# Kernel optimization log

Measured on AMD Instinct MI355X. Metric: run time of the kernel, lower is better.

The kernel has to match this reference:

```python
import jax, jax.numpy as jnp
import numpy as np

N = 50000        # nodes
E = 800000       # edges (avg degree 16)
F_NODE = 128     # node feature dim
F_EDGE = 8       # edge feature dim
H_ATT = 64       # attention hidden dim
H = 8            # attention heads
P = 16           # propagation dim per head (H*P = 128)


def setup_inputs() -> dict:
    key = jax.random.key(0)
    ks = jax.random.split(key, 16)
    s = lambda fan_in: 1.0 / np.sqrt(fan_in)
    return {
        "feat": jax.random.normal(ks[0], (N, F_NODE), jnp.float32),
        "feat_edge": jax.random.normal(ks[1], (E, F_EDGE), jnp.float32),
        "src": jax.random.randint(ks[2], (E,), 0, N, jnp.int32),
        "dst": jax.random.randint(ks[3], (E,), 0, N, jnp.int32),
        # attention MLPs (no bias), stored as [in, out]
        "w_att_src0": jax.random.normal(ks[4], (F_NODE, H_ATT), jnp.float32) * s(F_NODE),
        "w_att_src1": jax.random.normal(ks[5], (H_ATT, H), jnp.float32) * s(H_ATT),
        "w_att_dst0": jax.random.normal(ks[6], (F_NODE, H_ATT), jnp.float32) * s(F_NODE),
        "w_att_dst1": jax.random.normal(ks[7], (H_ATT, H), jnp.float32) * s(H_ATT),
        "w_att_edge0": jax.random.normal(ks[8], (F_EDGE, H_ATT), jnp.float32) * s(F_EDGE),
        "w_att_edge1": jax.random.normal(ks[9], (H_ATT, H), jnp.float32) * s(H_ATT),
        # propagation projections (single layer: Linear(F_NODE, H*P) with bias)
        "w_prop_src": jax.random.normal(ks[10], (F_NODE, H * P), jnp.float32) * s(F_NODE),
        "b_prop_src": jnp.zeros((H * P,), jnp.float32),
        "w_prop_dst": jax.random.normal(ks[11], (F_NODE, H * P), jnp.float32) * s(F_NODE),
        "b_prop_dst": jnp.zeros((H * P,), jnp.float32),
    }


def reference(feat, feat_edge, src, dst,
              w_att_src0, w_att_src1, w_att_dst0, w_att_dst1,
              w_att_edge0, w_att_edge1,
              w_prop_src, b_prop_src, w_prop_dst, b_prop_dst):
    relu = jax.nn.relu
    n = feat.shape[0]

    # propagation branch: [N, H*P] -> [N, H, P]
    prop_src = (feat @ w_prop_src + b_prop_src).reshape(n, H, P)
    prop_dst = (feat @ w_prop_dst + b_prop_dst).reshape(n, H, P)

    # attention MLPs -> per-node / per-edge head logits [*, H]
    a_src = relu(feat @ w_att_src0) @ w_att_src1          # [N, H]
    a_dst = relu(feat @ w_att_dst0) @ w_att_dst1          # [N, H]
    a_edge = relu(feat_edge @ w_att_edge0) @ w_att_edge1  # [E, H]

    # per-edge attention logit: relu(a_src[u] + a_dst[v] + a_edge)
    att = relu(a_src[src] + a_dst[dst] + a_edge)          # [E, H]

    # edge softmax over incoming edges of each destination node (per head)
    m = jax.ops.segment_max(att, dst, num_segments=n)     # [N, H]
    ex = jnp.exp(att - m[dst])                            # [E, H]
    denom = jax.ops.segment_sum(ex, dst, num_segments=n)  # [N, H]
    alpha = ex / jnp.maximum(denom[dst], 1e-16)           # [E, H]

    # message = prop_src[u] * alpha, sum-aggregate to destinations
    msg = prop_src[src] * alpha[:, :, None]               # [E, H, P]
    agg = jax.ops.segment_sum(msg, dst, num_segments=n)   # [N, H, P]

    # n_hiddens_agg == []: residual add of prop_dst
    return agg + prop_dst
```

## Files before the change

kernel.cpp:

```cpp
#include <hip/hip_runtime.h>
#include <hip/hip_bf16.h>

#define NODECAP 48
#define NPB 256
#define BCAP 4608
#define MAXBUCK 256
#define PART_CHUNK 1600
#define EPART_BLOCKS 500
#define SLICES 8

typedef __attribute__((ext_vector_type(8))) short bf16x8;
typedef __attribute__((ext_vector_type(4))) float f32x4;

static __device__ __forceinline__ short f2b(float f) {
    __hip_bfloat16 h = __float2bfloat16(f);
    return *reinterpret_cast<short*>(&h);
}
static __device__ __forceinline__ float b2f(unsigned short u) {
    union { unsigned int i; float f; } v; v.i = ((unsigned int)u) << 16; return v.f;
}

__global__ __launch_bounds__(256) void pack_w(
    const float* __restrict__ w_ps, const float* __restrict__ w_pd,
    const float* __restrict__ w_as0, const float* __restrict__ w_ad0,
    short* __restrict__ wp, short* __restrict__ wa, int* __restrict__ gcnt, int nbuck)
{
    const int idx = blockIdx.x * 256 + threadIdx.x;
    if (idx < 256 * 128) {
        const int c = idx >> 7, k = idx & 127;
        const float v = (c < 128) ? w_ps[(size_t)k * 128 + c] : w_pd[(size_t)k * 128 + (c - 128)];
        wp[idx] = f2b(v);
    } else if (idx < 256 * 128 + 128 * 128) {
        const int j = idx - 256 * 128;
        const int c = j >> 7, k = j & 127;
        const float v = (c < 64) ? w_as0[(size_t)k * 64 + c] : w_ad0[(size_t)k * 64 + (c - 64)];
        wa[j] = f2b(v);
    }
    if (idx < nbuck) gcnt[idx] = 0;
}

__global__ __launch_bounds__(256) void node_mfma(
    const float* __restrict__ feat,
    const short* __restrict__ wp, const short* __restrict__ wa,
    const float* __restrict__ b_ps, const float* __restrict__ b_pd,
    const float* __restrict__ w_as1, const float* __restrict__ w_ad1,
    short* __restrict__ prop_bf, short* __restrict__ pd_bf,
    short* __restrict__ a_src_bf, float* __restrict__ a_dst, int n)
{
    __shared__ unsigned char afb[64 * 256];
    __shared__ short ht[64][137];
    const int t = threadIdx.x;
    const int lane = t & 63;
    const int wid = t >> 6;
    const int l15 = lane & 15;
    const int l4 = lane >> 4;
    const int base = blockIdx.x * 64;

    #pragma unroll
    for (int i = 0; i < 4; ++i) {
        const int chunk = t + i * 256;
        const int row = chunk >> 4;
        const int kc = chunk & 15;
        const int grow = base + row;
        float f[8];
        if (grow < n) {
            const float4 v0 = *reinterpret_cast<const float4*>(feat + (size_t)grow * 128 + kc * 8);
            const float4 v1 = *reinterpret_cast<const float4*>(feat + (size_t)grow * 128 + kc * 8 + 4);
            f[0] = v0.x; f[1] = v0.y; f[2] = v0.z; f[3] = v0.w;
            f[4] = v1.x; f[5] = v1.y; f[6] = v1.z; f[7] = v1.w;
        } else {
            #pragma unroll
            for (int j = 0; j < 8; ++j) f[j] = 0.f;
        }
        short h8[8];
        #pragma unroll
        for (int j = 0; j < 8; ++j) h8[j] = f2b(f[j]);
        const int byte = (row * 256 + kc * 16) ^ ((row & 7) << 4);
        *reinterpret_cast<bf16x8*>(afb + byte) = *reinterpret_cast<const bf16x8*>(h8);
    }
    __syncthreads();

    {
        f32x4 acc[4][4] = {};
        for (int kk = 0; kk < 4; ++kk) {
            bf16x8 a[4], b[4];
            #pragma unroll
            for (int rt = 0; rt < 4; ++rt) {
                const int arow = rt * 16 + l15;
                const int ab = (arow * 256 + kk * 64 + l4 * 16) ^ ((arow & 7) << 4);
                a[rt] = *reinterpret_cast<const bf16x8*>(afb + ab);
            }
            #pragma unroll
            for (int c = 0; c < 4; ++c) {
                const int col = (wid * 4 + c) * 16 + l15;
                b[c] = *reinterpret_cast<const bf16x8*>(wp + (size_t)col * 128 + kk * 32 + l4 * 8);
            }
            #pragma unroll
            for (int rt = 0; rt < 4; ++rt)
                #pragma unroll
                for (int c = 0; c < 4; ++c)
                    acc[rt][c] = __builtin_amdgcn_mfma_f32_16x16x32_bf16(a[rt], b[c], acc[rt][c], 0, 0, 0);
        }
        #pragma unroll
        for (int c = 0; c < 4; ++c) {
            const int col = (wid * 4 + c) * 16 + l15;
            const bool sr = (col < 128);
            const float bias = sr ? b_ps[col] : b_pd[col - 128];
            short* dbase = sr ? (prop_bf + col) : (pd_bf + (col - 128));
            #pragma unroll
            for (int rt = 0; rt < 4; ++rt)
                #pragma unroll
                for (int r = 0; r < 4; ++r) {
                    const int row = base + rt * 16 + l4 * 4 + r;
                    if (row < n) dbase[(size_t)row * 128] = f2b(acc[rt][c][r] + bias);
                }
        }
    }

    {
        f32x4 acc[4][2] = {};
        for (int kk = 0; kk < 4; ++kk) {
            bf16x8 a[4], b[2];
            #pragma unroll
            for (int rt = 0; rt < 4; ++rt) {
                const int arow = rt * 16 + l15;
                const int ab = (arow * 256 + kk * 64 + l4 * 16) ^ ((arow & 7) << 4);
                a[rt] = *reinterpret_cast<const bf16x8*>(afb + ab);
            }
            #pragma unroll
            for (int c = 0; c < 2; ++c) {
                const int col = (wid * 2 + c) * 16 + l15;
                b[c] = *reinterpret_cast<const bf16x8*>(wa + (size_t)col * 128 + kk * 32 + l4 * 8);
            }
            #pragma unroll
            for (int rt = 0; rt < 4; ++rt)
                #pragma unroll
                for (int c = 0; c < 2; ++c)
                    acc[rt][c] = __builtin_amdgcn_mfma_f32_16x16x32_bf16(a[rt], b[c], acc[rt][c], 0, 0, 0);
        }
        #pragma unroll
        for (int c = 0; c < 2; ++c) {
            const int col = (wid * 2 + c) * 16 + l15;
            #pragma unroll
            for (int rt = 0; rt < 4; ++rt)
                #pragma unroll
                for (int r = 0; r < 4; ++r)
                    ht[rt * 16 + l4 * 4 + r][col] = f2b(fmaxf(acc[rt][c][r], 0.f));
        }
    }
    __syncthreads();

    #pragma unroll
    for (int o = 0; o < 4; ++o) {
        const int idx = t + o * 256;
        const int i = idx >> 4;
        const int hh = idx & 15;
        const bool is_src = (hh < 8);
        const int h = is_src ? hh : (hh - 8);
        const float* w1 = is_src ? w_as1 : w_ad1;
        const int jb = is_src ? 0 : 64;
        float acc = 0.f;
        #pragma unroll
        for (int j = 0; j < 64; ++j)
            acc += b2f((unsigned short)ht[i][jb + j]) * w1[j * 8 + h];
        const int row = base + i;
        if (row < n) {
            if (is_src) a_src_bf[(size_t)row * 8 + h] = f2b(acc);
            else        a_dst[(size_t)row * 8 + h] = acc;
        }
    }
}

__global__ __launch_bounds__(256) void edge_part(
    const int* __restrict__ src, const int* __restrict__ dst,
    const float* __restrict__ feat_edge,
    const float* __restrict__ w_e0, const float* __restrict__ w_e1,
    const short* __restrict__ a_src_bf,
    int* __restrict__ gcnt, int2* __restrict__ part, short* __restrict__ ax,
    int E, int nbuck)
{
    __shared__ int hist[MAXBUCK];
    __shared__ int cursor[MAXBUCK];
    __shared__ int dcache[PART_CHUNK];
    const int t = threadIdx.x;

    if (blockIdx.x < EPART_BLOCKS) {
        const int e0 = blockIdx.x * PART_CHUNK;
        const int e1 = min(e0 + PART_CHUNK, E);

        for (int i = t; i < nbuck; i += 256) hist[i] = 0;
        __syncthreads();
        for (int e = e0 + t; e < e1; e += 256) {
            const int d = dst[e];
            dcache[e - e0] = d;
            atomicAdd(&hist[d >> 8], 1);
        }
        __syncthreads();
        for (int i = t; i < nbuck; i += 256) {
            const int c = hist[i];
            cursor[i] = (c > 0) ? atomicAdd(&gcnt[i], c) : 0;
        }
        __syncthreads();
        for (int e = e0 + t; e < e1; e += 256) {
            const int d = dcache[e - e0];
            const int s = src[e];
            const int b = d >> 8;
            const int pos = atomicAdd(&cursor[b], 1);
            if (pos < BCAP)
                part[(size_t)b * BCAP + pos] = make_int2((e << 8) | (d & 255), s);
        }
        return;
    }

    const int e = (blockIdx.x - EPART_BLOCKS) * 256 + t;
    if (e >= E) return;

    float fe[8];
    const float4 v0 = *reinterpret_cast<const float4*>(feat_edge + (size_t)e * 8);
    const float4 v1 = *reinterpret_cast<const float4*>(feat_edge + (size_t)e * 8 + 4);
    fe[0] = v0.x; fe[1] = v0.y; fe[2] = v0.z; fe[3] = v0.w;
    fe[4] = v1.x; fe[5] = v1.y; fe[6] = v1.z; fe[7] = v1.w;

    float ae[8] = {};
    #pragma unroll 8
    for (int j = 0; j < 64; ++j) {
        float hj = 0.f;
        #pragma unroll
        for (int k = 0; k < 8; ++k) hj += fe[k] * w_e0[k * 64 + j];
        hj = fmaxf(hj, 0.f);
        #pragma unroll
        for (int hh = 0; hh < 8; ++hh) ae[hh] += hj * w_e1[j * 8 + hh];
    }

    const int s = src[e];
    const ushort4 as0 = *reinterpret_cast<const ushort4*>(a_src_bf + (size_t)s * 8);
    const ushort4 as1 = *reinterpret_cast<const ushort4*>(a_src_bf + (size_t)s * 8 + 4);
    short eb[8];
    eb[0] = f2b(ae[0] + b2f(as0.x)); eb[1] = f2b(ae[1] + b2f(as0.y));
    eb[2] = f2b(ae[2] + b2f(as0.z)); eb[3] = f2b(ae[3] + b2f(as0.w));
    eb[4] = f2b(ae[4] + b2f(as1.x)); eb[5] = f2b(ae[5] + b2f(as1.y));
    eb[6] = f2b(ae[6] + b2f(as1.z)); eb[7] = f2b(ae[7] + b2f(as1.w));
    *reinterpret_cast<uint4*>(ax + (size_t)e * 8) = *reinterpret_cast<const uint4*>(eb);
}

__global__ __launch_bounds__(256) void bucket_agg(
    const int2* __restrict__ part, const int* __restrict__ gcnt,
    const short* __restrict__ ax, const float* __restrict__ a_dst,
    const short* __restrict__ prop_bf, const short* __restrict__ pd_bf,
    float* __restrict__ out, int n)
{
    __shared__ int2  lists[32][NODECAP];
    __shared__ int   lcnt[32];
    __shared__ float adst_s[32][8];
    const int t = threadIdx.x;
    const int b = blockIdx.x >> 3;
    const int slice = blockIdx.x & 7;
    const int node0 = (b << 8) + (slice << 5);

    if (t < 32) lcnt[t] = 0;
    {
        const int r = t >> 3, h = t & 7;
        const int nd = node0 + r;
        adst_s[r][h] = (nd < n) ? a_dst[(size_t)nd * 8 + h] : 0.f;
    }
    __syncthreads();

    const int cnt = min(gcnt[b], BCAP);
    const int2* pb = part + (size_t)b * BCAP;
    for (int j = t; j < cnt; j += 256) {
        const int2 pr = pb[j];
        const int dlow = pr.x & 255;
        if ((dlow >> 5) == slice) {
            const int r = dlow & 31;
            const int slot = atomicAdd(&lcnt[r], 1);
            if (slot < NODECAP) lists[r][slot] = make_int2(pr.x >> 8, pr.y);
        }
    }
    __syncthreads();

    const int grp = t >> 5, l = t & 31;
    const int h = l >> 2, q = l & 3;

    for (int r = grp; r < 32; r += 8) {
        const int node = node0 + r;
        if (node >= n) continue;
        int deg = lcnt[r];
        if (deg > NODECAP) deg = NODECAP;
        const float adv = adst_s[r][h];

        float dsumv = 0.f;
        float4 acc = make_float4(0.f, 0.f, 0.f, 0.f);
        for (int j0 = 0; j0 < deg; j0 += 8) {
            float at[8]; float4 pv[8];
            #pragma unroll
            for (int u = 0; u < 8; ++u) {
                const int j = j0 + u;
                const bool act = (j < deg);
                const int2 pr = lists[r][act ? j : 0];
                at[u] = b2f((unsigned short)ax[(size_t)pr.x * 8 + h]);
                const ushort4 p = *reinterpret_cast<const ushort4*>(
                    prop_bf + (size_t)pr.y * 128 + h * 16 + q * 4);
                pv[u] = make_float4(b2f(p.x), b2f(p.y), b2f(p.z), b2f(p.w));
            }
            #pragma unroll
            for (int u = 0; u < 8; ++u) {
                const bool act = (j0 + u < deg);
                const float ex = act ? __expf(fmaxf(at[u] + adv, 0.f)) : 0.f;
                dsumv += ex;
                acc.x += ex * pv[u].x; acc.y += ex * pv[u].y;
                acc.z += ex * pv[u].z; acc.w += ex * pv[u].w;
            }
        }
        const float dinv = 1.f / fmaxf(dsumv, 1e-16f);

        const ushort4 pd = *reinterpret_cast<const ushort4*>(
            pd_bf + (size_t)node * 128 + h * 16 + q * 4);
        float4 o;
        o.x = b2f(pd.x) + acc.x * dinv; o.y = b2f(pd.y) + acc.y * dinv;
        o.z = b2f(pd.z) + acc.z * dinv; o.w = b2f(pd.w) + acc.w * dinv;
        *reinterpret_cast<float4*>(out + (size_t)node * 128 + h * 16 + q * 4) = o;
    }
}

extern "C" void kernel_launch(void* const* d_in, const int* in_sizes, int n_in,
                              void* d_out, int out_size, void* d_ws, size_t ws_size,
                              hipStream_t stream)
{
    const float* feat      = (const float*)d_in[0];
    const float* feat_edge = (const float*)d_in[1];
    const int*   src       = (const int*)d_in[2];
    const int*   dst       = (const int*)d_in[3];
    const float* w_as0     = (const float*)d_in[4];
    const float* w_as1     = (const float*)d_in[5];
    const float* w_ad0     = (const float*)d_in[6];
    const float* w_ad1     = (const float*)d_in[7];
    const float* w_e0      = (const float*)d_in[8];
    const float* w_e1      = (const float*)d_in[9];
    const float* w_ps      = (const float*)d_in[10];
    const float* b_ps      = (const float*)d_in[11];
    const float* w_pd      = (const float*)d_in[12];
    const float* b_pd      = (const float*)d_in[13];

    const int n = in_sizes[0] / 128;
    const int E = in_sizes[2];
    const int nbuck = (n + NPB - 1) / NPB;
    float* out = (float*)d_out;

    short* prop_bf = (short*)d_ws;
    short* pd_bf   = prop_bf + (size_t)n * 128;
    short* a_src_bf = pd_bf + (size_t)n * 128;
    float* a_dst = (float*)(a_src_bf + (size_t)n * 8);
    int*   gcnt  = (int*)(a_dst + (size_t)n * 8);
    int2*  part  = (int2*)(gcnt + ((nbuck + 1) & ~1));
    short* ax    = (short*)(part + (size_t)nbuck * BCAP);
    short* wp    = ax + (size_t)E * 8;
    short* wa    = wp + 256 * 128;

    pack_w<<<192, 256, 0, stream>>>(
        w_ps, w_pd, w_as0, w_ad0, wp, wa, gcnt, nbuck);

    node_mfma<<<(n + 63) / 64, 256, 0, stream>>>(
        feat, wp, wa, b_ps, b_pd, w_as1, w_ad1,
        prop_bf, pd_bf, a_src_bf, a_dst, n);

    const int axBlocks = (E + 255) / 256;
    edge_part<<<EPART_BLOCKS + axBlocks, 256, 0, stream>>>(
        src, dst, feat_edge, w_e0, w_e1, a_src_bf, gcnt, part, ax, E, nbuck);

    bucket_agg<<<nbuck * SLICES, 256, 0, stream>>>(
        part, gcnt, ax, a_dst, prop_bf, pd_bf, out, n);
}
```

Baseline: 150.4 us.

## Merge node projection and edge partition kernels into one launch

```diff
diff --git a/kernel.cpp b/kernel.cpp
--- a/kernel.cpp
+++ b/kernel.cpp
@@ -6,7 +6,6 @@
 #define BCAP 4608
 #define MAXBUCK 256
 #define PART_CHUNK 1600
-#define EPART_BLOCKS 500
 #define SLICES 8
 
 typedef __attribute__((ext_vector_type(8))) short bf16x8;
@@ -39,17 +38,80 @@
     if (idx < nbuck) gcnt[idx] = 0;
 }
 
-__global__ __launch_bounds__(256) void node_mfma(
+__global__ __launch_bounds__(256) void node_edge_part(
     const float* __restrict__ feat,
     const short* __restrict__ wp, const short* __restrict__ wa,
     const float* __restrict__ b_ps, const float* __restrict__ b_pd,
     const float* __restrict__ w_as1, const float* __restrict__ w_ad1,
     short* __restrict__ prop_bf, short* __restrict__ pd_bf,
-    short* __restrict__ a_src_bf, float* __restrict__ a_dst, int n)
+    short* __restrict__ a_src_bf, float* __restrict__ a_dst,
+    const int* __restrict__ src, const int* __restrict__ dst,
+    const float* __restrict__ feat_edge,
+    const float* __restrict__ w_e0, const float* __restrict__ w_e1,
+    int* __restrict__ gcnt, int2* __restrict__ part, short* __restrict__ ae,
+    int n, int E, int nbuck, int nodeB, int partB)
 {
-    __shared__ unsigned char afb[64 * 256];
-    __shared__ short ht[64][137];
+    __shared__ char smraw[64 * 256 + 64 * 137 * 2];
     const int t = threadIdx.x;
+
+    if (blockIdx.x >= nodeB + partB) {
+        const int e = (blockIdx.x - nodeB - partB) * 256 + t;
+        if (e >= E) return;
+        float fe[8];
+        const float4 v0 = *reinterpret_cast<const float4*>(feat_edge + (size_t)e * 8);
+        const float4 v1 = *reinterpret_cast<const float4*>(feat_edge + (size_t)e * 8 + 4);
+        fe[0] = v0.x; fe[1] = v0.y; fe[2] = v0.z; fe[3] = v0.w;
+        fe[4] = v1.x; fe[5] = v1.y; fe[6] = v1.z; fe[7] = v1.w;
+        float av[8] = {};
+        #pragma unroll 8
+        for (int j = 0; j < 64; ++j) {
+            float hj = 0.f;
+            #pragma unroll
+            for (int k = 0; k < 8; ++k) hj += fe[k] * w_e0[k * 64 + j];
+            hj = fmaxf(hj, 0.f);
+            #pragma unroll
+            for (int hh = 0; hh < 8; ++hh) av[hh] += hj * w_e1[j * 8 + hh];
+        }
+        short eb[8];
+        #pragma unroll
+        for (int hh = 0; hh < 8; ++hh) eb[hh] = f2b(av[hh]);
+        *reinterpret_cast<uint4*>(ae + (size_t)e * 8) = *reinterpret_cast<const uint4*>(eb);
+        return;
+    }
+
+    if (blockIdx.x >= nodeB) {
+        int* hist   = (int*)smraw;
+        int* cursor = hist + MAXBUCK;
+        int* dcache = cursor + MAXBUCK;
+        const int e0 = (blockIdx.x - nodeB) * PART_CHUNK;
+        const int e1 = min(e0 + PART_CHUNK, E);
+
+        for (int i = t; i < nbuck; i += 256) hist[i] = 0;
+        __syncthreads();
+        for (int e = e0 + t; e < e1; e += 256) {
+            const int d = dst[e];
+            dcache[e - e0] = d;
+            atomicAdd(&hist[d >> 8], 1);
+        }
+        __syncthreads();
+        for (int i = t; i < nbuck; i += 256) {
+            const int c = hist[i];
+            cursor[i] = (c > 0) ? atomicAdd(&gcnt[i], c) : 0;
+        }
+        __syncthreads();
+        for (int e = e0 + t; e < e1; e += 256) {
+            const int d = dcache[e - e0];
+            const int s = src[e];
+            const int b = d >> 8;
+            const int pos = atomicAdd(&cursor[b], 1);
+            if (pos < BCAP)
+                part[(size_t)b * BCAP + pos] = make_int2((e << 8) | (d & 255), s);
+        }
+        return;
+    }
+
+    unsigned char* afb = (unsigned char*)smraw;
+    short* ht = (short*)(smraw + 64 * 256);
     const int lane = t & 63;
     const int wid = t >> 6;
     const int l15 = lane & 15;
@@ -145,7 +207,7 @@
             for (int rt = 0; rt < 4; ++rt)
                 #pragma unroll
                 for (int r = 0; r < 4; ++r)
-                    ht[rt * 16 + l4 * 4 + r][col] = f2b(fmaxf(acc[rt][c][r], 0.f));
+                    ht[(rt * 16 + l4 * 4 + r) * 137 + col] = f2b(fmaxf(acc[rt][c][r], 0.f));
         }
     }
     __syncthreads();
@@ -162,7 +224,7 @@
         float acc = 0.f;
         #pragma unroll
         for (int j = 0; j < 64; ++j)
-            acc += b2f((unsigned short)ht[i][jb + j]) * w1[j * 8 + h];
+            acc += b2f((unsigned short)ht[i * 137 + jb + j]) * w1[j * 8 + h];
         const int row = base + i;
         if (row < n) {
             if (is_src) a_src_bf[(size_t)row * 8 + h] = f2b(acc);
@@ -171,81 +233,10 @@
     }
 }
 
-__global__ __launch_bounds__(256) void edge_part(
-    const int* __restrict__ src, const int* __restrict__ dst,
-    const float* __restrict__ feat_edge,
-    const float* __restrict__ w_e0, const float* __restrict__ w_e1,
-    const short* __restrict__ a_src_bf,
-    int* __restrict__ gcnt, int2* __restrict__ part, short* __restrict__ ax,
-    int E, int nbuck)
-{
-    __shared__ int hist[MAXBUCK];
-    __shared__ int cursor[MAXBUCK];
-    __shared__ int dcache[PART_CHUNK];
-    const int t = threadIdx.x;
-
-    if (blockIdx.x < EPART_BLOCKS) {
-        const int e0 = blockIdx.x * PART_CHUNK;
-        const int e1 = min(e0 + PART_CHUNK, E);
-
-        for (int i = t; i < nbuck; i += 256) hist[i] = 0;
-        __syncthreads();
-        for (int e = e0 + t; e < e1; e += 256) {
-            const int d = dst[e];
-            dcache[e - e0] = d;
-            atomicAdd(&hist[d >> 8], 1);
-        }
-        __syncthreads();
-        for (int i = t; i < nbuck; i += 256) {
-            const int c = hist[i];
-            cursor[i] = (c > 0) ? atomicAdd(&gcnt[i], c) : 0;
-        }
-        __syncthreads();
-        for (int e = e0 + t; e < e1; e += 256) {
-            const int d = dcache[e - e0];
-            const int s = src[e];
-            const int b = d >> 8;
-            const int pos = atomicAdd(&cursor[b], 1);
-            if (pos < BCAP)
-                part[(size_t)b * BCAP + pos] = make_int2((e << 8) | (d & 255), s);
-        }
-        return;
-    }
-
-    const int e = (blockIdx.x - EPART_BLOCKS) * 256 + t;
-    if (e >= E) return;
-
-    float fe[8];
-    const float4 v0 = *reinterpret_cast<const float4*>(feat_edge + (size_t)e * 8);
-    const float4 v1 = *reinterpret_cast<const float4*>(feat_edge + (size_t)e * 8 + 4);
-    fe[0] = v0.x; fe[1] = v0.y; fe[2] = v0.z; fe[3] = v0.w;
-    fe[4] = v1.x; fe[5] = v1.y; fe[6] = v1.z; fe[7] = v1.w;
-
-    float ae[8] = {};
-    #pragma unroll 8
-    for (int j = 0; j < 64; ++j) {
-        float hj = 0.f;
-        #pragma unroll
-        for (int k = 0; k < 8; ++k) hj += fe[k] * w_e0[k * 64 + j];
-        hj = fmaxf(hj, 0.f);
-        #pragma unroll
-        for (int hh = 0; hh < 8; ++hh) ae[hh] += hj * w_e1[j * 8 + hh];
-    }
-
-    const int s = src[e];
-    const ushort4 as0 = *reinterpret_cast<const ushort4*>(a_src_bf + (size_t)s * 8);
-    const ushort4 as1 = *reinterpret_cast<const ushort4*>(a_src_bf + (size_t)s * 8 + 4);
-    short eb[8];
-    eb[0] = f2b(ae[0] + b2f(as0.x)); eb[1] = f2b(ae[1] + b2f(as0.y));
-    eb[2] = f2b(ae[2] + b2f(as0.z)); eb[3] = f2b(ae[3] + b2f(as0.w));
-    eb[4] = f2b(ae[4] + b2f(as1.x)); eb[5] = f2b(ae[5] + b2f(as1.y));
-    eb[6] = f2b(ae[6] + b2f(as1.z)); eb[7] = f2b(ae[7] + b2f(as1.w));
-    *reinterpret_cast<uint4*>(ax + (size_t)e * 8) = *reinterpret_cast<const uint4*>(eb);
-}
-
 __global__ __launch_bounds__(256) void bucket_agg(
     const int2* __restrict__ part, const int* __restrict__ gcnt,
-    const short* __restrict__ ax, const float* __restrict__ a_dst,
+    const short* __restrict__ ae, const short* __restrict__ a_src_bf,
+    const float* __restrict__ a_dst,
     const short* __restrict__ prop_bf, const short* __restrict__ pd_bf,
     float* __restrict__ out, int n)
 {
@@ -297,7 +288,8 @@
                 const int j = j0 + u;
                 const bool act = (j < deg);
                 const int2 pr = lists[r][act ? j : 0];
-                at[u] = b2f((unsigned short)ax[(size_t)pr.x * 8 + h]);
+                at[u] = b2f((unsigned short)ae[(size_t)pr.x * 8 + h])
+                      + b2f((unsigned short)a_src_bf[(size_t)pr.y * 8 + h]);
                 const ushort4 p = *reinterpret_cast<const ushort4*>(
                     prop_bf + (size_t)pr.y * 128 + h * 16 + q * 4);
                 pv[u] = make_float4(b2f(p.x), b2f(p.y), b2f(p.z), b2f(p.w));
@@ -352,21 +344,22 @@
     float* a_dst = (float*)(a_src_bf + (size_t)n * 8);
     int*   gcnt  = (int*)(a_dst + (size_t)n * 8);
     int2*  part  = (int2*)(gcnt + ((nbuck + 1) & ~1));
-    short* ax    = (short*)(part + (size_t)nbuck * BCAP);
-    short* wp    = ax + (size_t)E * 8;
+    short* ae    = (short*)(part + (size_t)nbuck * BCAP);
+    short* wp    = ae + (size_t)E * 8;
     short* wa    = wp + 256 * 128;
 
     pack_w<<<192, 256, 0, stream>>>(
         w_ps, w_pd, w_as0, w_ad0, wp, wa, gcnt, nbuck);
 
-    node_mfma<<<(n + 63) / 64, 256, 0, stream>>>(
+    const int nodeB = (n + 63) / 64;
+    const int partB = (E + PART_CHUNK - 1) / PART_CHUNK;
+    const int aeB   = (E + 255) / 256;
+    node_edge_part<<<nodeB + partB + aeB, 256, 0, stream>>>(
         feat, wp, wa, b_ps, b_pd, w_as1, w_ad1,
-        prop_bf, pd_bf, a_src_bf, a_dst, n);
-
-    const int axBlocks = (E + 255) / 256;
-    edge_part<<<EPART_BLOCKS + axBlocks, 256, 0, stream>>>(
-        src, dst, feat_edge, w_e0, w_e1, a_src_bf, gcnt, part, ax, E, nbuck);
+        prop_bf, pd_bf, a_src_bf, a_dst,
+        src, dst, feat_edge, w_e0, w_e1,
+        gcnt, part, ae, n, E, nbuck, nodeB, partB);
 
     bucket_agg<<<nbuck * SLICES, 256, 0, stream>>>(
-        part, gcnt, ax, a_dst, prop_bf, pd_bf, out, n);
-}
+        part, gcnt, ae, a_src_bf, a_dst, prop_bf, pd_bf, out, n);
+}
```

After: 159.9 us. 6.4% more time.
